# Kernel optimization log

Measured on AMD Instinct MI355X. Metric: run time of the kernel, lower is better.

Reference implementation:

```python
import jax, jax.numpy as jnp
import numpy as np

CLIP_MAX = 1.0 / 1e-06  # torch.clip(1/d, max=1/1e-6)


def setup_inputs() -> dict:
    key = jax.random.key(0)
    k1, k2 = jax.random.split(key)
    base_features = jax.random.normal(k1, (4096, 512), dtype=jnp.float32)
    target_features = jax.random.normal(k2, (8192, 512), dtype=jnp.float32)
    return {"base_features": base_features, "target_features": target_features}


def _pairwise_euclidean(x, y):
    # Same math as sqrt(sum((x[:,None,:]-y[None,:,:])**2, -1)) but computed
    # via the expanded form to avoid materializing the (N,M,D) intermediate.
    x2 = jnp.sum(x * x, axis=1, keepdims=True)          # [N,1]
    y2 = jnp.sum(y * y, axis=1, keepdims=True).T        # [1,M]
    xy = x @ y.T                                        # [N,M]
    sq = jnp.maximum(x2 + y2 - 2.0 * xy, 0.0)
    return jnp.sqrt(sq)


def reference(base_features, target_features):
    # distance == 'euclidean' branch of SimilarityCalculatorFeatureOnly.forward
    dist = _pairwise_euclidean(base_features, target_features)   # [N,M]
    similarity = jnp.minimum(1.0 / dist, CLIP_MAX)                # clip at 1e6
    return (base_features, similarity)
```

## Files before the change

kernel.cpp:

```cpp
#include <hip/hip_runtime.h>
#include <hip/hip_bf16.h>
#include <stdint.h>

typedef short bf16x8 __attribute__((ext_vector_type(8)));
typedef float f32x4 __attribute__((ext_vector_type(4)));

#define D  512
#define NB 4096
#define NT 8192

__device__ __forceinline__ unsigned short f2bf(float f) {
    __hip_bfloat16 h = __float2bfloat16(f);
    return *reinterpret_cast<unsigned short*>(&h);
}

__global__ __launch_bounds__(256) void prep_kernel(
    const float* __restrict__ src, unsigned short* __restrict__ dst,
    float* __restrict__ norms, float* __restrict__ copy)
{
    const int row  = blockIdx.x * 4 + (threadIdx.x >> 6);
    const int lane = threadIdx.x & 63;
    const float4* rp = reinterpret_cast<const float4*>(src + (size_t)row * D);
    float4 v0 = rp[lane * 2];
    float4 v1 = rp[lane * 2 + 1];
    if (copy) {
        float4* cp = reinterpret_cast<float4*>(copy + (size_t)row * D);
        cp[lane * 2]     = v0;
        cp[lane * 2 + 1] = v1;
    }
    float s = v0.x*v0.x + v0.y*v0.y + v0.z*v0.z + v0.w*v0.w
            + v1.x*v1.x + v1.y*v1.y + v1.z*v1.z + v1.w*v1.w;
    union { unsigned short h[8]; int4 v; } u;
    u.h[0] = f2bf(v0.x); u.h[1] = f2bf(v0.y); u.h[2] = f2bf(v0.z); u.h[3] = f2bf(v0.w);
    u.h[4] = f2bf(v1.x); u.h[5] = f2bf(v1.y); u.h[6] = f2bf(v1.z); u.h[7] = f2bf(v1.w);
    reinterpret_cast<int4*>(dst + (size_t)row * D)[lane] = u.v;
    #pragma unroll
    for (int off = 32; off > 0; off >>= 1) s += __shfl_xor(s, off);
    if (lane == 0) norms[row] = s;
}

#define REGN(b, mat, ks) ((b) * 32768 + (mat) * 16384 + (ks) * 8192)

__global__ __launch_bounds__(512, 2) void gemm_sim_kernel(
    const unsigned short* __restrict__ X, const unsigned short* __restrict__ Y,
    const float* __restrict__ x2, const float* __restrict__ y2,
    float* __restrict__ out)
{
    __shared__ alignas(16) unsigned short lds[65536];

    const int tid  = threadIdx.x;
    const int lane = tid & 63;
    const int w    = tid >> 6;
    const int wr   = w >> 2;
    const int wc   = w & 3;

    const int bid = blockIdx.x;
    const int swz = (bid & 7) * 64 + (bid >> 3);
    const int rowBase = (swz & 15) * 256;
    const int colBase = (swz >> 4) * 256;

    const int rst = tid >> 2;
    const int gst = (tid & 3) ^ ((rst >> 1) & 3);
    const unsigned short* gA = X + (size_t)(rowBase + rst) * D + gst * 8;
    const unsigned short* gB = Y + (size_t)(colBase + rst) * D + gst * 8;
    const int ldst = w * 512;

    const int cread = ((lane >> 4) ^ ((lane >> 1) & 3)) * 8;
    const int aoff = (wr * 128 + (lane & 15)) * 32 + cread;
    const int boff = (wc * 64  + (lane & 15)) * 32 + cread;

    f32x4 acc[8][4] = {};
    bf16x8 bfr[4];

#define STAGE(BUF, MAT, KS, KT) do { \
    const unsigned short* _g = ((MAT) ? gB : gA) + (KT) * 64 + (KS) * 32; \
    const int _l = REGN(BUF, MAT, KS) + ldst; \
    __builtin_amdgcn_global_load_lds((const __attribute__((address_space(1))) void*)_g, \
        (__attribute__((address_space(3))) void*)(lds + _l), 16, 0, 0); \
    __builtin_amdgcn_global_load_lds((const __attribute__((address_space(1))) void*)(_g + 128 * D), \
        (__attribute__((address_space(3))) void*)(lds + _l + 4096), 16, 0, 0); \
} while (0)

#define PHASE(BUF, KS, MH, STG, CKPT) do { \
    bf16x8 _a[4]; \
    if ((MH) == 0) { \
        _Pragma("unroll") \
        for (int n = 0; n < 4; ++n) \
            bfr[n] = *(const bf16x8*)(lds + REGN(BUF, 1, KS) + boff + n * 512); \
    } \
    _Pragma("unroll") \
    for (int m = 0; m < 4; ++m) \
        _a[m] = *(const bf16x8*)(lds + REGN(BUF, 0, KS) + aoff + (MH) * 2048 + m * 512); \
    STG; \
    asm volatile("s_barrier" ::: "memory"); \
    asm volatile("s_waitcnt lgkmcnt(0)" ::: "memory"); \
    __builtin_amdgcn_s_setprio(1); \
    _Pragma("unroll") \
    for (int m = 0; m < 4; ++m) { \
        _Pragma("unroll") \
        for (int n = 0; n < 4; ++n) \
            acc[(MH) * 4 + m][n] = __builtin_amdgcn_mfma_f32_16x16x32_bf16(_a[m], bfr[n], acc[(MH) * 4 + m][n], 0, 0, 0); \
    } \
    __builtin_amdgcn_s_setprio(0); \
    CKPT; \
    asm volatile("s_barrier" ::: "memory"); \
} while (0)

    STAGE(0, 0, 0, 0); STAGE(0, 1, 0, 0); STAGE(0, 0, 1, 0); STAGE(0, 1, 1, 0);
    STAGE(1, 0, 0, 1); STAGE(1, 1, 0, 1);
    asm volatile("s_waitcnt vmcnt(4)" ::: "memory");
    asm volatile("s_barrier" ::: "memory");

#pragma unroll
    for (int j = 0; j < 4; ++j) {
        const int t1 = 2 * j + 1, t2 = 2 * j + 2, t3 = 2 * j + 3;
        PHASE(0, 0, 0, STAGE(1, 0, 1, t1), ((void)0));
        PHASE(0, 0, 1, STAGE(1, 1, 1, t1), ((void)0));
        PHASE(0, 1, 0, if (t2 < 8) STAGE(0, 0, 0, t2), ((void)0));
        PHASE(0, 1, 1, if (t2 < 8) STAGE(0, 1, 0, t2),
              if (j < 3) { asm volatile("s_waitcnt vmcnt(4)" ::: "memory"); }
              else       { asm volatile("s_waitcnt vmcnt(0)" ::: "memory"); });
        PHASE(1, 0, 0, if (t2 < 8) STAGE(0, 0, 1, t2), ((void)0));
        PHASE(1, 0, 1, if (t2 < 8) STAGE(0, 1, 1, t2), ((void)0));
        PHASE(1, 1, 0, if (t3 < 8) STAGE(1, 0, 0, t3), ((void)0));
        PHASE(1, 1, 1, if (t3 < 8) STAGE(1, 1, 0, t3),
              if (j < 3) { asm volatile("s_waitcnt vmcnt(4)" ::: "memory"); });
    }
#undef PHASE
#undef STAGE

    const int col0 = colBase + wc * 64 + (lane & 15);
    const int row0 = rowBase + wr * 128 + ((lane >> 4) << 2);
    #pragma unroll
    for (int mi = 0; mi < 8; ++mi) {
        const int rbase = row0 + (mi >> 2) * 64 + (mi & 3) * 16;
        #pragma unroll
        for (int q = 0; q < 4; ++q) {
            const int grow = rbase + q;
            const float xn = x2[grow];
            float* orow = out + (size_t)grow * NT;
            #pragma unroll
            for (int n = 0; n < 4; ++n) {
                const int gcol = col0 + n * 16;
                float sq = fmaxf(xn + y2[gcol] - 2.0f * acc[mi][n][q], 0.0f);
                orow[gcol] = fminf(rsqrtf(sq), 1.0e6f);
            }
        }
    }
}

extern "C" void kernel_launch(void* const* d_in, const int* in_sizes, int n_in,
                              void* d_out, int out_size, void* d_ws, size_t ws_size,
                              hipStream_t stream)
{
    const float* x = (const float*)d_in[0];
    const float* y = (const float*)d_in[1];
    float* out = (float*)d_out;
    char* ws = (char*)d_ws;

    unsigned short* xb = (unsigned short*)ws;
    unsigned short* yb = (unsigned short*)(ws + (4u << 20));
    float* x2 = (float*)(ws + (12u << 20));
    float* y2 = (float*)(ws + (12u << 20) + 4 * NB);

    prep_kernel<<<NB / 4, 256, 0, stream>>>(x, xb, x2, out);
    prep_kernel<<<NT / 4, 256, 0, stream>>>(y, yb, y2, nullptr);

    gemm_sim_kernel<<<512, 512, 0, stream>>>(xb, yb, x2, y2, out + (size_t)NB * D);
}
```

Before: 68.97 us.

## Process two column tiles per block, overlapping first epilogue with second tile's loads

Each GEMM block now computes two adjacent 256-column tiles in sequence, halving the grid to 256 blocks so every block is resident at once. The K-loop runs 16 steps instead of 8, and the first tile's epilogue runs while prefetches for the second tile are already in flight, hiding part of the store-heavy epilogue behind loads. Both prep kernels are merged into one launch. A new XCD-aware tile mapping is added, and the inline-asm barriers are replaced with the builtin. The trade-off is fewer blocks, so load balance across CUs may suffer.

Result: slower. 81.87 us (+18.7%).

```diff
diff --git a/kernel.cpp b/kernel.cpp
--- a/kernel.cpp
+++ b/kernel.cpp
@@ -15,15 +15,22 @@
 }
 
 __global__ __launch_bounds__(256) void prep_kernel(
-    const float* __restrict__ src, unsigned short* __restrict__ dst,
-    float* __restrict__ norms, float* __restrict__ copy)
+    const float* __restrict__ x, const float* __restrict__ y,
+    unsigned short* __restrict__ xb, unsigned short* __restrict__ yb,
+    float* __restrict__ x2, float* __restrict__ y2, float* __restrict__ copy)
 {
-    const int row  = blockIdx.x * 4 + (threadIdx.x >> 6);
+    const int grow = blockIdx.x * 4 + (threadIdx.x >> 6);
     const int lane = threadIdx.x & 63;
+    const bool isX = grow < NB;
+    const int row  = isX ? grow : grow - NB;
+    const float* src = isX ? x : y;
+    unsigned short* dst = isX ? xb : yb;
+    float* norms = isX ? x2 : y2;
+
     const float4* rp = reinterpret_cast<const float4*>(src + (size_t)row * D);
     float4 v0 = rp[lane * 2];
     float4 v1 = rp[lane * 2 + 1];
-    if (copy) {
+    if (isX) {
         float4* cp = reinterpret_cast<float4*>(copy + (size_t)row * D);
         cp[lane * 2]     = v0;
         cp[lane * 2 + 1] = v1;
@@ -54,15 +61,19 @@
     const int wr   = w >> 2;
     const int wc   = w & 3;
 
-    const int bid = blockIdx.x;
-    const int swz = (bid & 7) * 64 + (bid >> 3);
-    const int rowBase = (swz & 15) * 256;
-    const int colBase = (swz >> 4) * 256;
+    const int xcd = blockIdx.x & 7;
+    const int idx = blockIdx.x >> 3;
+    const int rowTile  = (xcd & 1) * 8 + (idx & 7);
+    const int colPair  = (xcd >> 1) * 4 + (idx >> 3);
+    const int rowBase  = rowTile * 256;
+    const int colBase0 = colPair * 512;
+    const int colBase1 = colBase0 + 256;
 
     const int rst = tid >> 2;
     const int gst = (tid & 3) ^ ((rst >> 1) & 3);
-    const unsigned short* gA = X + (size_t)(rowBase + rst) * D + gst * 8;
-    const unsigned short* gB = Y + (size_t)(colBase + rst) * D + gst * 8;
+    const unsigned short* gA  = X + (size_t)(rowBase  + rst) * D + gst * 8;
+    const unsigned short* gB0 = Y + (size_t)(colBase0 + rst) * D + gst * 8;
+    const unsigned short* gB1 = Y + (size_t)(colBase1 + rst) * D + gst * 8;
     const int ldst = w * 512;
 
     const int cread = ((lane >> 4) ^ ((lane >> 1) & 3)) * 8;
@@ -73,7 +84,8 @@
     bf16x8 bfr[4];
 
 #define STAGE(BUF, MAT, KS, KT) do { \
-    const unsigned short* _g = ((MAT) ? gB : gA) + (KT) * 64 + (KS) * 32; \
+    const unsigned short* _g = ((MAT) ? (((KT) < 8) ? gB0 : gB1) : gA) \
+                               + ((KT) & 7) * 64 + (KS) * 32; \
     const int _l = REGN(BUF, MAT, KS) + ldst; \
     __builtin_amdgcn_global_load_lds((const __attribute__((address_space(1))) void*)_g, \
         (__attribute__((address_space(3))) void*)(lds + _l), 16, 0, 0); \
@@ -92,7 +104,7 @@
     for (int m = 0; m < 4; ++m) \
         _a[m] = *(const bf16x8*)(lds + REGN(BUF, 0, KS) + aoff + (MH) * 2048 + m * 512); \
     STG; \
-    asm volatile("s_barrier" ::: "memory"); \
+    __builtin_amdgcn_s_barrier(); \
     asm volatile("s_waitcnt lgkmcnt(0)" ::: "memory"); \
     __builtin_amdgcn_s_setprio(1); \
     _Pragma("unroll") \
@@ -103,50 +115,62 @@
     } \
     __builtin_amdgcn_s_setprio(0); \
     CKPT; \
-    asm volatile("s_barrier" ::: "memory"); \
+    __builtin_amdgcn_s_barrier(); \
+} while (0)
+
+#define EPILOGUE(CB) do { \
+    const int col0 = (CB) + wc * 64 + (lane & 15); \
+    const int row0 = rowBase + wr * 128 + ((lane >> 4) << 2); \
+    _Pragma("unroll") \
+    for (int mi = 0; mi < 8; ++mi) { \
+        const int rbase = row0 + (mi >> 2) * 64 + (mi & 3) * 16; \
+        _Pragma("unroll") \
+        for (int q = 0; q < 4; ++q) { \
+            const int grow = rbase + q; \
+            const float xn = x2[grow]; \
+            float* orow = out + (size_t)grow * NT; \
+            _Pragma("unroll") \
+            for (int n = 0; n < 4; ++n) { \
+                const int gcol = col0 + n * 16; \
+                float sq = fmaxf(xn + y2[gcol] - 2.0f * acc[mi][n][q], 0.0f); \
+                orow[gcol] = fminf(rsqrtf(sq), 1.0e6f); \
+            } \
+        } \
+    } \
 } while (0)
 
     STAGE(0, 0, 0, 0); STAGE(0, 1, 0, 0); STAGE(0, 0, 1, 0); STAGE(0, 1, 1, 0);
     STAGE(1, 0, 0, 1); STAGE(1, 1, 0, 1);
     asm volatile("s_waitcnt vmcnt(4)" ::: "memory");
-    asm volatile("s_barrier" ::: "memory");
+    __builtin_amdgcn_s_barrier();
 
 #pragma unroll
-    for (int j = 0; j < 4; ++j) {
+    for (int j = 0; j < 8; ++j) {
         const int t1 = 2 * j + 1, t2 = 2 * j + 2, t3 = 2 * j + 3;
         PHASE(0, 0, 0, STAGE(1, 0, 1, t1), ((void)0));
         PHASE(0, 0, 1, STAGE(1, 1, 1, t1), ((void)0));
-        PHASE(0, 1, 0, if (t2 < 8) STAGE(0, 0, 0, t2), ((void)0));
-        PHASE(0, 1, 1, if (t2 < 8) STAGE(0, 1, 0, t2),
-              if (j < 3) { asm volatile("s_waitcnt vmcnt(4)" ::: "memory"); }
+        PHASE(0, 1, 0, if (t2 < 16) STAGE(0, 0, 0, t2), ((void)0));
+        PHASE(0, 1, 1, if (t2 < 16) STAGE(0, 1, 0, t2),
+              if (j < 7) { asm volatile("s_waitcnt vmcnt(4)" ::: "memory"); }
               else       { asm volatile("s_waitcnt vmcnt(0)" ::: "memory"); });
-        PHASE(1, 0, 0, if (t2 < 8) STAGE(0, 0, 1, t2), ((void)0));
-        PHASE(1, 0, 1, if (t2 < 8) STAGE(0, 1, 1, t2), ((void)0));
-        PHASE(1, 1, 0, if (t3 < 8) STAGE(1, 0, 0, t3), ((void)0));
-        PHASE(1, 1, 1, if (t3 < 8) STAGE(1, 1, 0, t3),
-              if (j < 3) { asm volatile("s_waitcnt vmcnt(4)" ::: "memory"); });
+        PHASE(1, 0, 0, if (t2 < 16) STAGE(0, 0, 1, t2), ((void)0));
+        PHASE(1, 0, 1, if (t2 < 16) STAGE(0, 1, 1, t2), ((void)0));
+        PHASE(1, 1, 0, if (t3 < 16) STAGE(1, 0, 0, t3), ((void)0));
+        PHASE(1, 1, 1, if (t3 < 16) STAGE(1, 1, 0, t3),
+              if (j < 7) { asm volatile("s_waitcnt vmcnt(4)" ::: "memory"); });
+        if (j == 3) {
+            EPILOGUE(colBase0);
+            #pragma unroll
+            for (int mi = 0; mi < 8; ++mi)
+                #pragma unroll
+                for (int n = 0; n < 4; ++n)
+                    acc[mi][n] = (f32x4){0.f, 0.f, 0.f, 0.f};
+        }
     }
 #undef PHASE
 #undef STAGE
 
-    const int col0 = colBase + wc * 64 + (lane & 15);
-    const int row0 = rowBase + wr * 128 + ((lane >> 4) << 2);
-    #pragma unroll
-    for (int mi = 0; mi < 8; ++mi) {
-        const int rbase = row0 + (mi >> 2) * 64 + (mi & 3) * 16;
-        #pragma unroll
-        for (int q = 0; q < 4; ++q) {
-            const int grow = rbase + q;
-            const float xn = x2[grow];
-            float* orow = out + (size_t)grow * NT;
-            #pragma unroll
-            for (int n = 0; n < 4; ++n) {
-                const int gcol = col0 + n * 16;
-                float sq = fmaxf(xn + y2[gcol] - 2.0f * acc[mi][n][q], 0.0f);
-                orow[gcol] = fminf(rsqrtf(sq), 1.0e6f);
-            }
-        }
-    }
+    EPILOGUE(colBase1);
 }
 
 extern "C" void kernel_launch(void* const* d_in, const int* in_sizes, int n_in,
@@ -163,8 +187,6 @@
     float* x2 = (float*)(ws + (12u << 20));
     float* y2 = (float*)(ws + (12u << 20) + 4 * NB);
 
-    prep_kernel<<<NB / 4, 256, 0, stream>>>(x, xb, x2, out);
-    prep_kernel<<<NT / 4, 256, 0, stream>>>(y, yb, y2, nullptr);
-
-    gemm_sim_kernel<<<512, 512, 0, stream>>>(xb, yb, x2, y2, out + (size_t)NB * D);
+    prep_kernel<<<(NB + NT) / 4, 256, 0, stream>>>(x, y, xb, yb, x2, y2, out);
+    gemm_sim_kernel<<<256, 512, 0, stream>>>(xb, yb, x2, y2, out + (size_t)NB * D);
 }
```

## Shrink GEMM tile to 128x256 with 4 waves and merge prep launches

Applied to the files above, without the earlier changes.

The GEMM block tile goes from 256x256 with 8 waves and 128 KB of LDS to 128x256 with 4 waves and 48 KB of LDS, giving 1024 blocks. The K step drops to 32 with a double-buffered A/B pipeline, and the XCD-aware block mapping is reworked to match. The two prep kernels are also merged into one launch covering both inputs. This aims at better occupancy and load balance across CUs and one less launch, at the cost of lower per-block data reuse and more global traffic for the A/B tiles.

Result: faster. 62.11 us (-9.9%).

```diff
diff --git a/kernel.cpp b/kernel.cpp
--- a/kernel.cpp
+++ b/kernel.cpp
@@ -15,15 +15,22 @@
 }
 
 __global__ __launch_bounds__(256) void prep_kernel(
-    const float* __restrict__ src, unsigned short* __restrict__ dst,
-    float* __restrict__ norms, float* __restrict__ copy)
+    const float* __restrict__ x, const float* __restrict__ y,
+    unsigned short* __restrict__ xb, unsigned short* __restrict__ yb,
+    float* __restrict__ x2, float* __restrict__ y2, float* __restrict__ copy)
 {
-    const int row  = blockIdx.x * 4 + (threadIdx.x >> 6);
+    const int grow = blockIdx.x * 4 + (threadIdx.x >> 6);
     const int lane = threadIdx.x & 63;
+    const bool isX = grow < NB;
+    const int row  = isX ? grow : grow - NB;
+    const float* src = isX ? x : y;
+    unsigned short* dst = isX ? xb : yb;
+    float* norms = isX ? x2 : y2;
+
     const float4* rp = reinterpret_cast<const float4*>(src + (size_t)row * D);
     float4 v0 = rp[lane * 2];
     float4 v1 = rp[lane * 2 + 1];
-    if (copy) {
+    if (isX) {
         float4* cp = reinterpret_cast<float4*>(copy + (size_t)row * D);
         cp[lane * 2]     = v0;
         cp[lane * 2 + 1] = v1;
@@ -39,60 +46,62 @@
     if (lane == 0) norms[row] = s;
 }
 
-#define REGN(b, mat, ks) ((b) * 32768 + (mat) * 16384 + (ks) * 8192)
-
-__global__ __launch_bounds__(512, 2) void gemm_sim_kernel(
+__global__ __launch_bounds__(256, 2) void gemm_sim_kernel(
     const unsigned short* __restrict__ X, const unsigned short* __restrict__ Y,
     const float* __restrict__ x2, const float* __restrict__ y2,
     float* __restrict__ out)
 {
-    __shared__ alignas(16) unsigned short lds[65536];
+    __shared__ alignas(16) unsigned short lds[24576];
 
-    const int tid  = threadIdx.x;
-    const int lane = tid & 63;
-    const int w    = tid >> 6;
-    const int wr   = w >> 2;
-    const int wc   = w & 3;
+    const int t    = threadIdx.x;
+    const int lane = t & 63;
+    const int w    = t >> 6;
 
     const int bid = blockIdx.x;
-    const int swz = (bid & 7) * 64 + (bid >> 3);
-    const int rowBase = (swz & 15) * 256;
-    const int colBase = (swz >> 4) * 256;
+    const int xcd = bid & 7;
+    const int idx = bid >> 3;
+    const int rowBase = ((xcd & 3) * 8 + (idx & 7)) * 128;
+    const int colBase = ((xcd >> 2) * 16 + (idx >> 3)) * 256;
 
-    const int rst = tid >> 2;
-    const int gst = (tid & 3) ^ ((rst >> 1) & 3);
-    const unsigned short* gA = X + (size_t)(rowBase + rst) * D + gst * 8;
-    const unsigned short* gB = Y + (size_t)(colBase + rst) * D + gst * 8;
-    const int ldst = w * 512;
+    const int swz = ((t & 3) ^ ((t >> 3) & 3)) * 8;
+    const unsigned short* gA = X + (size_t)(rowBase + (t >> 2)) * D + swz;
+    const unsigned short* gB = Y + (size_t)(colBase + (t >> 2)) * D + swz;
 
     const int cread = ((lane >> 4) ^ ((lane >> 1) & 3)) * 8;
-    const int aoff = (wr * 128 + (lane & 15)) * 32 + cread;
-    const int boff = (wc * 64  + (lane & 15)) * 32 + cread;
+    const int aoff = (lane & 15) * 32 + cread;
+    const int boff = 4096 + (w * 64 + (lane & 15)) * 32 + cread;
 
     f32x4 acc[8][4] = {};
     bf16x8 bfr[4];
 
-#define STAGE(BUF, MAT, KS, KT) do { \
-    const unsigned short* _g = ((MAT) ? gB : gA) + (KT) * 64 + (KS) * 32; \
-    const int _l = REGN(BUF, MAT, KS) + ldst; \
-    __builtin_amdgcn_global_load_lds((const __attribute__((address_space(1))) void*)_g, \
-        (__attribute__((address_space(3))) void*)(lds + _l), 16, 0, 0); \
-    __builtin_amdgcn_global_load_lds((const __attribute__((address_space(1))) void*)(_g + 128 * D), \
-        (__attribute__((address_space(3))) void*)(lds + _l + 4096), 16, 0, 0); \
+#define STAGE_A(BUF, KT) do { \
+    _Pragma("unroll") \
+    for (int L = 0; L < 2; ++L) \
+        __builtin_amdgcn_global_load_lds( \
+            (const __attribute__((address_space(1))) void*)(gA + (size_t)L * 64 * D + (KT) * 32), \
+            (__attribute__((address_space(3))) void*)(lds + (BUF) * 12288 + t * 8 + L * 2048), 16, 0, 0); \
 } while (0)
 
-#define PHASE(BUF, KS, MH, STG, CKPT) do { \
+#define STAGE_B(BUF, KT) do { \
+    _Pragma("unroll") \
+    for (int L = 0; L < 4; ++L) \
+        __builtin_amdgcn_global_load_lds( \
+            (const __attribute__((address_space(1))) void*)(gB + (size_t)L * 64 * D + (KT) * 32), \
+            (__attribute__((address_space(3))) void*)(lds + (BUF) * 12288 + 4096 + t * 8 + L * 2048), 16, 0, 0); \
+} while (0)
+
+#define PHASE(BUF, MH, STG, CKPT) do { \
     bf16x8 _a[4]; \
     if ((MH) == 0) { \
         _Pragma("unroll") \
         for (int n = 0; n < 4; ++n) \
-            bfr[n] = *(const bf16x8*)(lds + REGN(BUF, 1, KS) + boff + n * 512); \
+            bfr[n] = *(const bf16x8*)(lds + (BUF) * 12288 + boff + n * 512); \
     } \
     _Pragma("unroll") \
     for (int m = 0; m < 4; ++m) \
-        _a[m] = *(const bf16x8*)(lds + REGN(BUF, 0, KS) + aoff + (MH) * 2048 + m * 512); \
+        _a[m] = *(const bf16x8*)(lds + (BUF) * 12288 + aoff + (MH) * 2048 + m * 512); \
     STG; \
-    asm volatile("s_barrier" ::: "memory"); \
+    __builtin_amdgcn_s_barrier(); \
     asm volatile("s_waitcnt lgkmcnt(0)" ::: "memory"); \
     __builtin_amdgcn_s_setprio(1); \
     _Pragma("unroll") \
@@ -103,34 +112,29 @@
     } \
     __builtin_amdgcn_s_setprio(0); \
     CKPT; \
-    asm volatile("s_barrier" ::: "memory"); \
+    __builtin_amdgcn_s_barrier(); \
 } while (0)
 
-    STAGE(0, 0, 0, 0); STAGE(0, 1, 0, 0); STAGE(0, 0, 1, 0); STAGE(0, 1, 1, 0);
-    STAGE(1, 0, 0, 1); STAGE(1, 1, 0, 1);
+    STAGE_B(0, 0); STAGE_A(0, 0); STAGE_B(1, 1);
     asm volatile("s_waitcnt vmcnt(4)" ::: "memory");
-    asm volatile("s_barrier" ::: "memory");
+    __builtin_amdgcn_s_barrier();
 
 #pragma unroll
-    for (int j = 0; j < 4; ++j) {
-        const int t1 = 2 * j + 1, t2 = 2 * j + 2, t3 = 2 * j + 3;
-        PHASE(0, 0, 0, STAGE(1, 0, 1, t1), ((void)0));
-        PHASE(0, 0, 1, STAGE(1, 1, 1, t1), ((void)0));
-        PHASE(0, 1, 0, if (t2 < 8) STAGE(0, 0, 0, t2), ((void)0));
-        PHASE(0, 1, 1, if (t2 < 8) STAGE(0, 1, 0, t2),
-              if (j < 3) { asm volatile("s_waitcnt vmcnt(4)" ::: "memory"); }
+    for (int j = 0; j < 8; ++j) {
+        PHASE(0, 0, STAGE_A(1, 2 * j + 1), ((void)0));
+        PHASE(0, 1, if (j < 7) STAGE_B(0, 2 * j + 2),
+              if (j < 7) { asm volatile("s_waitcnt vmcnt(4)" ::: "memory"); }
               else       { asm volatile("s_waitcnt vmcnt(0)" ::: "memory"); });
-        PHASE(1, 0, 0, if (t2 < 8) STAGE(0, 0, 1, t2), ((void)0));
-        PHASE(1, 0, 1, if (t2 < 8) STAGE(0, 1, 1, t2), ((void)0));
-        PHASE(1, 1, 0, if (t3 < 8) STAGE(1, 0, 0, t3), ((void)0));
-        PHASE(1, 1, 1, if (t3 < 8) STAGE(1, 1, 0, t3),
-              if (j < 3) { asm volatile("s_waitcnt vmcnt(4)" ::: "memory"); });
+        PHASE(1, 0, if (j < 7) STAGE_A(0, 2 * j + 2), ((void)0));
+        PHASE(1, 1, if (j < 7) STAGE_B(1, 2 * j + 3),
+              if (j < 7) { asm volatile("s_waitcnt vmcnt(4)" ::: "memory"); });
     }
 #undef PHASE
-#undef STAGE
+#undef STAGE_A
+#undef STAGE_B
 
-    const int col0 = colBase + wc * 64 + (lane & 15);
-    const int row0 = rowBase + wr * 128 + ((lane >> 4) << 2);
+    const int col0 = colBase + w * 64 + (lane & 15);
+    const int row0 = rowBase + ((lane >> 4) << 2);
     #pragma unroll
     for (int mi = 0; mi < 8; ++mi) {
         const int rbase = row0 + (mi >> 2) * 64 + (mi & 3) * 16;
@@ -163,8 +167,6 @@
     float* x2 = (float*)(ws + (12u << 20));
     float* y2 = (float*)(ws + (12u << 20) + 4 * NB);
 
-    prep_kernel<<<NB / 4, 256, 0, stream>>>(x, xb, x2, out);
-    prep_kernel<<<NT / 4, 256, 0, stream>>>(y, yb, y2, nullptr);
-
-    gemm_sim_kernel<<<512, 512, 0, stream>>>(xb, yb, x2, y2, out + (size_t)NB * D);
+    prep_kernel<<<(NB + NT) / 4, 256, 0, stream>>>(x, y, xb, yb, x2, y2, out);
+    gemm_sim_kernel<<<1024, 256, 0, stream>>>(xb, yb, x2, y2, out + (size_t)NB * D);
 }
```
